# Kernel tuning notes

Hardware: AMD Instinct MI355X
Metric: run time of the kernel (lower is better)

The kernel has to match this reference:

```python
import jax, jax.numpy as jnp
import numpy as np

EMBED_DIM = 1024
NUM_HEADS = 16
HEAD_DIM = EMBED_DIM // NUM_HEADS


def setup_inputs() -> dict:
    key = jax.random.key(0)
    k1, k2, k3, k4 = jax.random.split(key, 4)
    B, N, C = 4, 4096, EMBED_DIM
    x = jax.random.normal(k1, (B, N, C), dtype=jnp.float32)
    scale = 1.0 / np.sqrt(C)
    W_qkv = jax.random.normal(k2, (C, 3 * C), dtype=jnp.float32) * scale
    W_out = jax.random.normal(k3, (C, C), dtype=jnp.float32) * scale
    b_out = jax.random.normal(k4, (C,), dtype=jnp.float32) * 0.01
    return {"x": x, "W_qkv": W_qkv, "W_out": W_out, "b_out": b_out}


def reference(x, W_qkv, W_out, b_out):
    B, N, C = x.shape
    H, D = NUM_HEADS, HEAD_DIM
    qkv = (x @ W_qkv).reshape(B, N, 3, H, D)
    qkv = jnp.transpose(qkv, (2, 0, 3, 1, 4))  # (3, B, H, N, D)
    q, k, v = qkv[0], qkv[1], qkv[2]
    q = jax.nn.elu(q) + 1.0
    k = jax.nn.elu(k) + 1.0
    kv = jnp.einsum('bhnd,bhne->bhde', k, v)          # (B,H,D,D)
    num = jnp.einsum('bhnd,bhde->bhne', q, kv)        # (B,H,N,D)
    normalizer = jnp.einsum('bhnd,bhd->bhn', q, k.sum(axis=2))
    out = num / (normalizer[..., None] + 1e-6)
    out = jnp.transpose(out, (0, 2, 1, 3)).reshape(B, N, C)
    return out @ W_out + b_out
```

## Files before the change

### kernel.cpp

```cpp
#include <hip/hip_runtime.h>
#include <hip/hip_bf16.h>

using bf16x8 = __bf16 __attribute__((ext_vector_type(8)));
using f32x4  = float  __attribute__((ext_vector_type(4)));
using u16x8  = unsigned short __attribute__((ext_vector_type(8)));
using u16x4  = unsigned short __attribute__((ext_vector_type(4)));

__device__ __forceinline__ unsigned short f2bf(float f) {
  unsigned u = __builtin_bit_cast(unsigned, f);
  u += 0x7fffu + ((u >> 16) & 1u);
  return (unsigned short)(u >> 16);
}
__device__ __forceinline__ float bf2f(unsigned short h) {
  return __builtin_bit_cast(float, (unsigned)h << 16);
}

__device__ __forceinline__ void gload16(const void* g, void* l) {
  __builtin_amdgcn_global_load_lds(
      (const __attribute__((address_space(1))) void*)g,
      (__attribute__((address_space(3))) void*)l, 16, 0, 0);
}

__device__ __forceinline__ void barrier_raw() {
  asm volatile("" ::: "memory");
  __builtin_amdgcn_s_barrier();
  asm volatile("" ::: "memory");
}
#define LGKM0() asm volatile("s_waitcnt lgkmcnt(0)" ::: "memory")
#define VMC6()  asm volatile("s_waitcnt vmcnt(6)" ::: "memory")
#define VMC0()  asm volatile("s_waitcnt vmcnt(0)" ::: "memory")

__global__ __launch_bounds__(256) void conv_f32_bf16(const float* __restrict__ in,
                                                     unsigned short* __restrict__ out, int n) {
  int stride = gridDim.x * 256 * 4;
  for (int i = (blockIdx.x * 256 + threadIdx.x) * 4; i < n; i += stride) {
    float4 v = *reinterpret_cast<const float4*>(in + i);
    u16x4 o = { f2bf(v.x), f2bf(v.y), f2bf(v.z), f2bf(v.w) };
    *reinterpret_cast<u16x4*>(out + i) = o;
  }
}

__global__ __launch_bounds__(256) void transpose_f32_bf16(const float* __restrict__ in,
                                                          unsigned short* __restrict__ out,
                                                          int R, int C) {
  __shared__ float t[64][65];
  int c0 = blockIdx.x * 64, r0 = blockIdx.y * 64;
  int lx = threadIdx.x & 63, ly = threadIdx.x >> 6;
#pragma unroll
  for (int i = 0; i < 16; ++i) {
    int r = ly * 16 + i;
    t[r][lx] = in[(size_t)(r0 + r) * C + c0 + lx];
  }
  __syncthreads();
#pragma unroll
  for (int i = 0; i < 16; ++i) {
    int c = ly * 16 + i;
    out[(size_t)(c0 + c) * R + r0 + lx] = f2bf(t[lx][c]);
  }
}

__device__ __forceinline__ void gemm256_mainloop(
    const unsigned short* __restrict__ A, const unsigned short* __restrict__ Bt,
    int brow, int bcol, char* lds, f32x4 (&acc)[8][4]) {
  constexpr int NT = 16;
  const int tid  = threadIdx.x;
  const int lane = tid & 63;
  const int w    = tid >> 6;
  const int wr   = w >> 2, wc = w & 3;
  const int lr   = lane & 15, kg = lane >> 4;

  const int o0 = tid * 16;
  const int o1 = 8192 + tid * 16;
  const int p0 = o0 ^ (((o0 >> 7) & 7) << 4);
  const int p1 = o1 ^ (((o1 >> 7) & 7) << 4);
  const int off0 = (p0 >> 7) * 2048 + (p0 & 127);
  const int off1 = (p1 >> 7) * 2048 + (p1 & 127);
  const int wq = w << 10;

  const int xr  = (lr & 7) << 4;
  const int ck0 = (kg * 16) ^ xr;
  const int ck1 = (64 + kg * 16) ^ xr;
  const int aoff = wr * 16384 + lr * 128;
  const int boff = 32768 + (wc >> 1) * 16384 + (wc & 1) * 8192 + lr * 128;

  auto STAGE = [&](const unsigned short* G, int rowbase, int t, int region) {
    const char* gb = (const char*)(G + (size_t)rowbase * 1024 + t * 64);
    char* lb = lds + region + wq;
    gload16(gb + off0, lb);
    gload16(gb + off1, lb + 8192);
  };

  STAGE(Bt, bcol,       0, 32768);
  STAGE(Bt, bcol + 128, 0, 32768 + 16384);
  STAGE(A,  brow,       0, 0);
  STAGE(A,  brow + 128, 0, 16384);
  STAGE(Bt, bcol,       1, 65536 + 32768);
  STAGE(Bt, bcol + 128, 1, 65536 + 32768 + 16384);
  STAGE(A,  brow,       1, 65536);
  VMC6();
  barrier_raw();

  bf16x8 aF[4][2], bF[4][2];
  for (int t = 0; t < NT; ++t) {
    const int bufo  = (t & 1) << 16;
    const int nbufo = bufo ^ 65536;
    const char* LA = lds + bufo + aoff;
    const char* LB = lds + bufo + boff;

#pragma unroll
    for (int n = 0; n < 2; ++n) {
      bF[n][0] = __builtin_bit_cast(bf16x8, *(const u16x8*)(LB + n * 2048 + ck0));
      bF[n][1] = __builtin_bit_cast(bf16x8, *(const u16x8*)(LB + n * 2048 + ck1));
    }
#pragma unroll
    for (int m = 0; m < 4; ++m) {
      aF[m][0] = __builtin_bit_cast(bf16x8, *(const u16x8*)(LA + m * 2048 + ck0));
      aF[m][1] = __builtin_bit_cast(bf16x8, *(const u16x8*)(LA + m * 2048 + ck1));
    }
    if (t + 1 < NT) STAGE(A, brow + 128, t + 1, nbufo + 16384);
    barrier_raw();
    LGKM0();
    __builtin_amdgcn_s_setprio(1);
#pragma unroll
    for (int kk = 0; kk < 2; ++kk)
#pragma unroll
      for (int m = 0; m < 4; ++m)
#pragma unroll
        for (int n = 0; n < 2; ++n)
          acc[m][n] = __builtin_amdgcn_mfma_f32_16x16x32_bf16(aF[m][kk], bF[n][kk], acc[m][n], 0, 0, 0);
    __builtin_amdgcn_s_setprio(0);
    barrier_raw();

#pragma unroll
    for (int n = 2; n < 4; ++n) {
      bF[n][0] = __builtin_bit_cast(bf16x8, *(const u16x8*)(LB + n * 2048 + ck0));
      bF[n][1] = __builtin_bit_cast(bf16x8, *(const u16x8*)(LB + n * 2048 + ck1));
    }
    barrier_raw();
    LGKM0();
    __builtin_amdgcn_s_setprio(1);
#pragma unroll
    for (int kk = 0; kk < 2; ++kk)
#pragma unroll
      for (int m = 0; m < 4; ++m)
#pragma unroll
        for (int n = 2; n < 4; ++n)
          acc[m][n] = __builtin_amdgcn_mfma_f32_16x16x32_bf16(aF[m][kk], bF[n][kk], acc[m][n], 0, 0, 0);
    __builtin_amdgcn_s_setprio(0);
    barrier_raw();

#pragma unroll
    for (int m = 0; m < 4; ++m) {
      aF[m][0] = __builtin_bit_cast(bf16x8, *(const u16x8*)(LA + (m + 4) * 2048 + ck0));
      aF[m][1] = __builtin_bit_cast(bf16x8, *(const u16x8*)(LA + (m + 4) * 2048 + ck1));
    }
    if (t + 2 < NT) STAGE(Bt, bcol, t + 2, bufo + 32768);
    barrier_raw();
    LGKM0();
    __builtin_amdgcn_s_setprio(1);
#pragma unroll
    for (int kk = 0; kk < 2; ++kk)
#pragma unroll
      for (int m = 0; m < 4; ++m)
#pragma unroll
        for (int n = 2; n < 4; ++n)
          acc[m + 4][n] = __builtin_amdgcn_mfma_f32_16x16x32_bf16(aF[m][kk], bF[n][kk], acc[m + 4][n], 0, 0, 0);
    __builtin_amdgcn_s_setprio(0);
    barrier_raw();

    if (t + 2 < NT) {
      STAGE(Bt, bcol + 128, t + 2, bufo + 32768 + 16384);
      STAGE(A,  brow,       t + 2, bufo);
    }
    barrier_raw();
    __builtin_amdgcn_s_setprio(1);
#pragma unroll
    for (int kk = 0; kk < 2; ++kk)
#pragma unroll
      for (int m = 0; m < 4; ++m)
#pragma unroll
        for (int n = 0; n < 2; ++n)
          acc[m + 4][n] = __builtin_amdgcn_mfma_f32_16x16x32_bf16(aF[m][kk], bF[n][kk], acc[m + 4][n], 0, 0, 0);
    __builtin_amdgcn_s_setprio(0);
    if (t + 2 < NT) { VMC6(); } else { VMC0(); }
    barrier_raw();
  }
}

__global__ __launch_bounds__(512, 2) void gemm_qkv(
    const unsigned short* __restrict__ xbf, const unsigned short* __restrict__ wt,
    unsigned short* __restrict__ q, unsigned short* __restrict__ k, unsigned short* __restrict__ v) {
  __shared__ __align__(16) char lds[131072];
  f32x4 acc[8][4] = {};
  const int bid = blockIdx.x;
  const int r = bid & 7, i = bid >> 3;
  const int tm = r * 8 + (i & 7);
  const int tn = i >> 3;
  const int brow = tm * 256, bcol = tn * 256;
  gemm256_mainloop(xbf, wt, brow, bcol, lds, acc);

  const int lane = threadIdx.x & 63, w = threadIdx.x >> 6;
  const int wr = w >> 2, wc = w & 3;
  const int lr = lane & 15, kg = lane >> 4;
#pragma unroll
  for (int m = 0; m < 8; ++m)
#pragma unroll
    for (int n = 0; n < 4; ++n)
#pragma unroll
      for (int rr = 0; rr < 4; ++rr) {
        int grow = brow + wr * 128 + m * 16 + kg * 4 + rr;
        int gcol = bcol + wc * 64 + n * 16 + lr;
        float val = acc[m][n][rr];
        int tt = gcol >> 10;
        int h = (gcol >> 6) & 15;
        int d = gcol & 63;
        int b = grow >> 12, s = grow & 4095;
        size_t idx = ((size_t)(b * 16 + h) * 4096 + s) * 64 + d;
        if (tt < 2) {
          val = val > 0.f ? val + 1.f : __expf(val);
          (tt == 0 ? q : k)[idx] = f2bf(val);
        } else {
          v[idx] = f2bf(val);
        }
      }
}

__global__ __launch_bounds__(512, 2) void gemm_out(
    const unsigned short* __restrict__ attn, const unsigned short* __restrict__ wt,
    const float* __restrict__ bias, float* __restrict__ out) {
  __shared__ __align__(16) char lds[131072];
  f32x4 acc[8][4] = {};
  const int bid = blockIdx.x;
  const int r = bid & 7, i = bid >> 3;
  const int tm = r * 8 + (i & 7);
  const int tn = i >> 3;
  const int brow = tm * 256, bcol = tn * 256;
  gemm256_mainloop(attn, wt, brow, bcol, lds, acc);

  const int lane = threadIdx.x & 63, w = threadIdx.x >> 6;
  const int wr = w >> 2, wc = w & 3;
  const int lr = lane & 15, kg = lane >> 4;
#pragma unroll
  for (int m = 0; m < 8; ++m)
#pragma unroll
    for (int n = 0; n < 4; ++n)
#pragma unroll
      for (int rr = 0; rr < 4; ++rr) {
        int grow = brow + wr * 128 + m * 16 + kg * 4 + rr;
        int gcol = bcol + wc * 64 + n * 16 + lr;
        out[(size_t)grow * 1024 + gcol] = acc[m][n][rr] + bias[gcol];
      }
}

__global__ __launch_bounds__(256) void kv_kernel(
    const unsigned short* __restrict__ k, const unsigned short* __restrict__ v,
    float* __restrict__ kv, float* __restrict__ ksum) {
  const int bid = blockIdx.x;
  const int bh = bid >> 3, chunk = bid & 7;
  const unsigned short* kb = k + (size_t)bh * 4096 * 64 + chunk * 512 * 64;
  const unsigned short* vb = v + (size_t)bh * 4096 * 64 + chunk * 512 * 64;
  __shared__ unsigned short ks[64 * 64];
  __shared__ unsigned short vs[64 * 64];
  const int tid = threadIdx.x;
  const int ty = tid >> 4, tx = tid & 15;
  float acc[4][4] = {};
  float ksacc[4] = {};
  for (int t = 0; t < 8; ++t) {
    const unsigned short* ksrc = kb + t * 4096;
    const unsigned short* vsrc = vb + t * 4096;
    *reinterpret_cast<u16x8*>(&ks[tid * 8])        = *reinterpret_cast<const u16x8*>(ksrc + tid * 8);
    *reinterpret_cast<u16x8*>(&ks[2048 + tid * 8]) = *reinterpret_cast<const u16x8*>(ksrc + 2048 + tid * 8);
    *reinterpret_cast<u16x8*>(&vs[tid * 8])        = *reinterpret_cast<const u16x8*>(vsrc + tid * 8);
    *reinterpret_cast<u16x8*>(&vs[2048 + tid * 8]) = *reinterpret_cast<const u16x8*>(vsrc + 2048 + tid * 8);
    __syncthreads();
#pragma unroll 4
    for (int nn = 0; nn < 64; ++nn) {
      u16x4 ku = *reinterpret_cast<const u16x4*>(&ks[nn * 64 + ty * 4]);
      u16x4 vu = *reinterpret_cast<const u16x4*>(&vs[nn * 64 + tx * 4]);
      float kd[4], ve[4];
#pragma unroll
      for (int i = 0; i < 4; ++i) { kd[i] = bf2f(ku[i]); ve[i] = bf2f(vu[i]); }
#pragma unroll
      for (int i = 0; i < 4; ++i) ksacc[i] += kd[i];
#pragma unroll
      for (int i = 0; i < 4; ++i)
#pragma unroll
        for (int j = 0; j < 4; ++j) acc[i][j] += kd[i] * ve[j];
    }
    __syncthreads();
  }
  float* kvb = kv + (size_t)bh * 4096;
#pragma unroll
  for (int i = 0; i < 4; ++i)
#pragma unroll
    for (int j = 0; j < 4; ++j)
      atomicAdd(&kvb[(tx * 4 + j) * 64 + ty * 4 + i], acc[i][j]);
  if (tx == 0) {
#pragma unroll
    for (int i = 0; i < 4; ++i) atomicAdd(&ksum[bh * 64 + ty * 4 + i], ksacc[i]);
  }
}

__global__ __launch_bounds__(256) void num_kernel(
    const unsigned short* __restrict__ q, const float* __restrict__ kv,
    const float* __restrict__ ksum, unsigned short* __restrict__ attn) {
  const int bid = blockIdx.x;
  const int bh = bid >> 6, sblk = bid & 63;
  const int b = bh >> 4, h = bh & 15;
  __shared__ unsigned short kvs[64 * 72];
  __shared__ float ksum_s[64];
  __shared__ float norm_s[64];
  const int tid = threadIdx.x;
  const float* kvb = kv + (size_t)bh * 4096;
#pragma unroll
  for (int r = 0; r < 4; ++r) {
    int e = r * 1024 + tid * 4;
    float4 f = *reinterpret_cast<const float4*>(&kvb[e]);
    int row = e >> 6, col = e & 63;
    u16x4 o = { f2bf(f.x), f2bf(f.y), f2bf(f.z), f2bf(f.w) };
    *reinterpret_cast<u16x4*>(&kvs[row * 72 + col]) = o;
  }
  if (tid < 16) {
    float4 f = *reinterpret_cast<const float4*>(&ksum[bh * 64 + tid * 4]);
    ksum_s[tid * 4 + 0] = f.x; ksum_s[tid * 4 + 1] = f.y;
    ksum_s[tid * 4 + 2] = f.z; ksum_s[tid * 4 + 3] = f.w;
  }
  __syncthreads();

  const int lane = tid & 63, w = tid >> 6;
  const int lr = lane & 15, kg = lane >> 4;
  const int s0 = sblk * 64 + w * 16;
  const unsigned short* qrow = q + ((size_t)bh * 4096 + s0 + lr) * 64 + kg * 8;
  u16x8 a0u = *reinterpret_cast<const u16x8*>(qrow);
  u16x8 a1u = *reinterpret_cast<const u16x8*>(qrow + 32);
  bf16x8 a0 = __builtin_bit_cast(bf16x8, a0u);
  bf16x8 a1 = __builtin_bit_cast(bf16x8, a1u);

  float p = 0.f;
#pragma unroll
  for (int j = 0; j < 8; ++j) {
    p += bf2f(a0u[j]) * ksum_s[kg * 8 + j];
    p += bf2f(a1u[j]) * ksum_s[32 + kg * 8 + j];
  }
  p += __shfl_xor(p, 16);
  p += __shfl_xor(p, 32);
  if (kg == 0) norm_s[w * 16 + lr] = p;

  f32x4 accs[4];
#pragma unroll
  for (int jf = 0; jf < 4; ++jf) {
    u16x8 b0u = *reinterpret_cast<const u16x8*>(&kvs[(jf * 16 + lr) * 72 + kg * 8]);
    u16x8 b1u = *reinterpret_cast<const u16x8*>(&kvs[(jf * 16 + lr) * 72 + 32 + kg * 8]);
    f32x4 c = {0.f, 0.f, 0.f, 0.f};
    c = __builtin_amdgcn_mfma_f32_16x16x32_bf16(a0, __builtin_bit_cast(bf16x8, b0u), c, 0, 0, 0);
    c = __builtin_amdgcn_mfma_f32_16x16x32_bf16(a1, __builtin_bit_cast(bf16x8, b1u), c, 0, 0, 0);
    accs[jf] = c;
  }
  float dn[4];
#pragma unroll
  for (int r = 0; r < 4; ++r) dn[r] = norm_s[w * 16 + kg * 4 + r] + 1e-6f;

  unsigned short* ab = attn + (size_t)b * 4096 * 1024 + h * 64;
#pragma unroll
  for (int jf = 0; jf < 4; ++jf)
#pragma unroll
    for (int r = 0; r < 4; ++r) {
      int s = s0 + kg * 4 + r;
      int e2 = jf * 16 + lr;
      ab[(size_t)s * 1024 + e2] = f2bf(accs[jf][r] / dn[r]);
    }
}

extern "C" void kernel_launch(void* const* d_in, const int* in_sizes, int n_in,
                              void* d_out, int out_size, void* d_ws, size_t ws_size,
                              hipStream_t stream) {
  const float* x     = (const float*)d_in[0];
  const float* W_qkv = (const float*)d_in[1];
  const float* W_out = (const float*)d_in[2];
  const float* b_out = (const float*)d_in[3];
  float* out = (float*)d_out;

  unsigned short* xbf   = (unsigned short*)d_ws;
  unsigned short* attnb = xbf;
  unsigned short* wqkvT = xbf + 16777216;
  unsigned short* woutT = wqkvT + 3145728;
  unsigned short* qb    = woutT + 1048576;
  unsigned short* kb    = qb + 16777216;
  unsigned short* vb    = kb + 16777216;
  float* kvw            = (float*)(vb + 16777216);
  float* ksumw          = kvw + 262144;

  conv_f32_bf16<<<2048, 256, 0, stream>>>(x, xbf, 16777216);
  transpose_f32_bf16<<<dim3(48, 16), 256, 0, stream>>>(W_qkv, wqkvT, 1024, 3072);
  transpose_f32_bf16<<<dim3(16, 16), 256, 0, stream>>>(W_out, woutT, 1024, 1024);
  hipMemsetAsync(kvw, 0, (262144 + 4096) * sizeof(float), stream);
  gemm_qkv<<<768, 512, 0, stream>>>(xbf, wqkvT, qb, kb, vb);
  kv_kernel<<<512, 256, 0, stream>>>(kb, vb, kvw, ksumw);
  num_kernel<<<4096, 256, 0, stream>>>(qb, kvw, ksumw, attnb);
  gemm_out<<<256, 512, 0, stream>>>(attnb, woutT, b_out, out);
}
```

Measured before the change: 261.2 us.

## Restructure GEMM mainloop into two-barrier ping-pong schedule with register double-buffering

```diff
diff --git a/kernel.cpp b/kernel.cpp
--- a/kernel.cpp
+++ b/kernel.cpp
@@ -26,9 +26,8 @@
   __builtin_amdgcn_s_barrier();
   asm volatile("" ::: "memory");
 }
-#define LGKM0() asm volatile("s_waitcnt lgkmcnt(0)" ::: "memory")
-#define VMC6()  asm volatile("s_waitcnt vmcnt(6)" ::: "memory")
-#define VMC0()  asm volatile("s_waitcnt vmcnt(0)" ::: "memory")
+#define VMC4() asm volatile("s_waitcnt vmcnt(4)" ::: "memory")
+#define VMC0() asm volatile("s_waitcnt vmcnt(0)" ::: "memory")
 
 __global__ __launch_bounds__(256) void conv_f32_bf16(const float* __restrict__ in,
                                                      unsigned short* __restrict__ out, int n) {
@@ -90,100 +89,84 @@
     gload16(gb + off1, lb + 8192);
   };
 
+  bf16x8 aQ[4][2], aR[4][2], bL0[2][2], bL1[2][2], bH[2][2];
+
+  auto READ_A = [&](bf16x8 (&dst)[4][2], int bufo, int mb) {
+#pragma unroll
+    for (int m = 0; m < 4; ++m) {
+      const char* p = lds + bufo + aoff + (mb + m) * 2048;
+      dst[m][0] = __builtin_bit_cast(bf16x8, *(const u16x8*)(p + ck0));
+      dst[m][1] = __builtin_bit_cast(bf16x8, *(const u16x8*)(p + ck1));
+    }
+  };
+  auto READ_B = [&](bf16x8 (&dst)[2][2], int bufo, int nb) {
+#pragma unroll
+    for (int n = 0; n < 2; ++n) {
+      const char* p = lds + bufo + boff + (nb + n) * 2048;
+      dst[n][0] = __builtin_bit_cast(bf16x8, *(const u16x8*)(p + ck0));
+      dst[n][1] = __builtin_bit_cast(bf16x8, *(const u16x8*)(p + ck1));
+    }
+  };
+  auto MFMA_Q = [&](int mb, int nb, bf16x8 (&Af)[4][2], bf16x8 (&Bf)[2][2]) {
+    __builtin_amdgcn_s_setprio(1);
+#pragma unroll
+    for (int kk = 0; kk < 2; ++kk)
+#pragma unroll
+      for (int m = 0; m < 4; ++m)
+#pragma unroll
+        for (int n = 0; n < 2; ++n)
+          acc[mb + m][nb + n] =
+              __builtin_amdgcn_mfma_f32_16x16x32_bf16(Af[m][kk], Bf[n][kk], acc[mb + m][nb + n], 0, 0, 0);
+    __builtin_amdgcn_s_setprio(0);
+  };
+
   STAGE(Bt, bcol,       0, 32768);
-  STAGE(Bt, bcol + 128, 0, 32768 + 16384);
+  STAGE(Bt, bcol + 128, 0, 49152);
   STAGE(A,  brow,       0, 0);
   STAGE(A,  brow + 128, 0, 16384);
   STAGE(Bt, bcol,       1, 65536 + 32768);
-  STAGE(Bt, bcol + 128, 1, 65536 + 32768 + 16384);
-  STAGE(A,  brow,       1, 65536);
-  VMC6();
+  STAGE(Bt, bcol + 128, 1, 65536 + 49152);
+  VMC4();
   barrier_raw();
-
-  bf16x8 aF[4][2], bF[4][2];
-  for (int t = 0; t < NT; ++t) {
-    const int bufo  = (t & 1) << 16;
-    const int nbufo = bufo ^ 65536;
-    const char* LA = lds + bufo + aoff;
-    const char* LB = lds + bufo + boff;
-
-#pragma unroll
-    for (int n = 0; n < 2; ++n) {
-      bF[n][0] = __builtin_bit_cast(bf16x8, *(const u16x8*)(LB + n * 2048 + ck0));
-      bF[n][1] = __builtin_bit_cast(bf16x8, *(const u16x8*)(LB + n * 2048 + ck1));
-    }
-#pragma unroll
-    for (int m = 0; m < 4; ++m) {
-      aF[m][0] = __builtin_bit_cast(bf16x8, *(const u16x8*)(LA + m * 2048 + ck0));
-      aF[m][1] = __builtin_bit_cast(bf16x8, *(const u16x8*)(LA + m * 2048 + ck1));
-    }
-    if (t + 1 < NT) STAGE(A, brow + 128, t + 1, nbufo + 16384);
+  READ_A(aQ, 0, 0);
+  READ_B(bL0, 0, 0);
+
+  for (int t = 0; t < NT; t += 2) {
+    if (t + 1 < NT) { STAGE(A, brow, t + 1, 65536); STAGE(A, brow + 128, t + 1, 65536 + 16384); }
+    READ_B(bH, 0, 2);
+    MFMA_Q(0, 0, aQ, bL0);
+    READ_A(aR, 0, 4);
+    MFMA_Q(0, 2, aQ, bH);
+    MFMA_Q(4, 2, aR, bH);
     barrier_raw();
-    LGKM0();
-    __builtin_amdgcn_s_setprio(1);
-#pragma unroll
-    for (int kk = 0; kk < 2; ++kk)
-#pragma unroll
-      for (int m = 0; m < 4; ++m)
-#pragma unroll
-        for (int n = 0; n < 2; ++n)
-          acc[m][n] = __builtin_amdgcn_mfma_f32_16x16x32_bf16(aF[m][kk], bF[n][kk], acc[m][n], 0, 0, 0);
-    __builtin_amdgcn_s_setprio(0);
+    if (t + 2 < NT) {
+      STAGE(Bt, bcol, t + 2, 32768); STAGE(Bt, bcol + 128, t + 2, 49152);
+      VMC4();
+    } else if (t + 1 < NT) {
+      VMC0();
+    }
     barrier_raw();
-
-#pragma unroll
-    for (int n = 2; n < 4; ++n) {
-      bF[n][0] = __builtin_bit_cast(bf16x8, *(const u16x8*)(LB + n * 2048 + ck0));
-      bF[n][1] = __builtin_bit_cast(bf16x8, *(const u16x8*)(LB + n * 2048 + ck1));
-    }
-    barrier_raw();
-    LGKM0();
-    __builtin_amdgcn_s_setprio(1);
-#pragma unroll
-    for (int kk = 0; kk < 2; ++kk)
-#pragma unroll
-      for (int m = 0; m < 4; ++m)
-#pragma unroll
-        for (int n = 2; n < 4; ++n)
-          acc[m][n] = __builtin_amdgcn_mfma_f32_16x16x32_bf16(aF[m][kk], bF[n][kk], acc[m][n], 0, 0, 0);
-    __builtin_amdgcn_s_setprio(0);
-    barrier_raw();
-
-#pragma unroll
-    for (int m = 0; m < 4; ++m) {
-      aF[m][0] = __builtin_bit_cast(bf16x8, *(const u16x8*)(LA + (m + 4) * 2048 + ck0));
-      aF[m][1] = __builtin_bit_cast(bf16x8, *(const u16x8*)(LA + (m + 4) * 2048 + ck1));
-    }
-    if (t + 2 < NT) STAGE(Bt, bcol, t + 2, bufo + 32768);
-    barrier_raw();
-    LGKM0();
-    __builtin_amdgcn_s_setprio(1);
-#pragma unroll
-    for (int kk = 0; kk < 2; ++kk)
-#pragma unroll
-      for (int m = 0; m < 4; ++m)
-#pragma unroll
-        for (int n = 2; n < 4; ++n)
-          acc[m + 4][n] = __builtin_amdgcn_mfma_f32_16x16x32_bf16(aF[m][kk], bF[n][kk], acc[m + 4][n], 0, 0, 0);
-    __builtin_amdgcn_s_setprio(0);
-    barrier_raw();
-
-    if (t + 2 < NT) {
-      STAGE(Bt, bcol + 128, t + 2, bufo + 32768 + 16384);
-      STAGE(A,  brow,       t + 2, bufo);
-    }
-    barrier_raw();
-    __builtin_amdgcn_s_setprio(1);
-#pragma unroll
-    for (int kk = 0; kk < 2; ++kk)
-#pragma unroll
-      for (int m = 0; m < 4; ++m)
-#pragma unroll
-        for (int n = 0; n < 2; ++n)
-          acc[m + 4][n] = __builtin_amdgcn_mfma_f32_16x16x32_bf16(aF[m][kk], bF[n][kk], acc[m + 4][n], 0, 0, 0);
-    __builtin_amdgcn_s_setprio(0);
-    if (t + 2 < NT) { VMC6(); } else { VMC0(); }
-    barrier_raw();
+    if (t + 1 < NT) { READ_A(aQ, 65536, 0); READ_B(bL1, 65536, 0); }
+    MFMA_Q(4, 0, aR, bL0);
+
+    if (t + 1 < NT) {
+      if (t + 2 < NT) { STAGE(A, brow, t + 2, 0); STAGE(A, brow + 128, t + 2, 16384); }
+      READ_B(bH, 65536, 2);
+      MFMA_Q(0, 0, aQ, bL1);
+      READ_A(aR, 65536, 4);
+      MFMA_Q(0, 2, aQ, bH);
+      MFMA_Q(4, 2, aR, bH);
+      barrier_raw();
+      if (t + 3 < NT) {
+        STAGE(Bt, bcol, t + 3, 65536 + 32768); STAGE(Bt, bcol + 128, t + 3, 65536 + 49152);
+        VMC4();
+      } else if (t + 2 < NT) {
+        VMC0();
+      }
+      barrier_raw();
+      if (t + 2 < NT) { READ_A(aQ, 0, 0); READ_B(bL0, 0, 0); }
+      MFMA_Q(4, 0, aR, bL1);
+    }
   }
 }
 
```

Result: slower. 320.0 us (+22.5%).

## Compute K^T V with MFMA and write partial sums instead of atomics

Applied to the files above, without the earlier changes.

```diff
diff --git a/kernel.cpp b/kernel.cpp
--- a/kernel.cpp
+++ b/kernel.cpp
@@ -91,11 +91,11 @@
   };
 
   STAGE(Bt, bcol,       0, 32768);
-  STAGE(Bt, bcol + 128, 0, 32768 + 16384);
+  STAGE(Bt, bcol + 128, 0, 49152);
   STAGE(A,  brow,       0, 0);
   STAGE(A,  brow + 128, 0, 16384);
   STAGE(Bt, bcol,       1, 65536 + 32768);
-  STAGE(Bt, bcol + 128, 1, 65536 + 32768 + 16384);
+  STAGE(Bt, bcol + 128, 1, 65536 + 49152);
   STAGE(A,  brow,       1, 65536);
   VMC6();
   barrier_raw();
@@ -169,7 +169,7 @@
     barrier_raw();
 
     if (t + 2 < NT) {
-      STAGE(Bt, bcol + 128, t + 2, bufo + 32768 + 16384);
+      STAGE(Bt, bcol + 128, t + 2, bufo + 49152);
       STAGE(A,  brow,       t + 2, bufo);
     }
     barrier_raw();
@@ -252,58 +252,93 @@
       }
 }
 
-__global__ __launch_bounds__(256) void kv_kernel(
+__global__ __launch_bounds__(256) void kv_mfma(
     const unsigned short* __restrict__ k, const unsigned short* __restrict__ v,
-    float* __restrict__ kv, float* __restrict__ ksum) {
+    float* __restrict__ kv_part, float* __restrict__ ksum_part) {
   const int bid = blockIdx.x;
-  const int bh = bid >> 3, chunk = bid & 7;
-  const unsigned short* kb = k + (size_t)bh * 4096 * 64 + chunk * 512 * 64;
-  const unsigned short* vb = v + (size_t)bh * 4096 * 64 + chunk * 512 * 64;
-  __shared__ unsigned short ks[64 * 64];
-  __shared__ unsigned short vs[64 * 64];
-  const int tid = threadIdx.x;
-  const int ty = tid >> 4, tx = tid & 15;
-  float acc[4][4] = {};
-  float ksacc[4] = {};
-  for (int t = 0; t < 8; ++t) {
-    const unsigned short* ksrc = kb + t * 4096;
-    const unsigned short* vsrc = vb + t * 4096;
-    *reinterpret_cast<u16x8*>(&ks[tid * 8])        = *reinterpret_cast<const u16x8*>(ksrc + tid * 8);
-    *reinterpret_cast<u16x8*>(&ks[2048 + tid * 8]) = *reinterpret_cast<const u16x8*>(ksrc + 2048 + tid * 8);
-    *reinterpret_cast<u16x8*>(&vs[tid * 8])        = *reinterpret_cast<const u16x8*>(vsrc + tid * 8);
-    *reinterpret_cast<u16x8*>(&vs[2048 + tid * 8]) = *reinterpret_cast<const u16x8*>(vsrc + 2048 + tid * 8);
+  const int bh = bid >> 1, half = bid & 1;
+  const size_t nbase = (size_t)bh * 4096 + half * 2048;
+  __shared__ unsigned short kt[64 * 72];
+  __shared__ unsigned short vt[64 * 72];
+  const int tid  = threadIdx.x;
+  const int lane = tid & 63, w = tid >> 6;
+  const int lr = lane & 15, kg = lane >> 4;
+  const int srow = w * 16 + (lane >> 2);
+  const int sd   = (lane & 3) * 16;
+
+  f32x4 acc[4] = {{0.f,0.f,0.f,0.f},{0.f,0.f,0.f,0.f},{0.f,0.f,0.f,0.f},{0.f,0.f,0.f,0.f}};
+  f32x4 ks[4]  = {{0.f,0.f,0.f,0.f},{0.f,0.f,0.f,0.f},{0.f,0.f,0.f,0.f},{0.f,0.f,0.f,0.f}};
+  const u16x8 onesu = { 0x3F80,0x3F80,0x3F80,0x3F80,0x3F80,0x3F80,0x3F80,0x3F80 };
+  const bf16x8 aone = __builtin_bit_cast(bf16x8, onesu);
+
+  const int arow = w * 16 + lr;
+  const int axor = ((arow >> 3) & 7) << 3;
+  const unsigned short* aB[2];
+  aB[0] = vt + arow * 72 + ((kg * 8) ^ axor);
+  aB[1] = vt + arow * 72 + ((32 + kg * 8) ^ axor);
+  const unsigned short* bB[4][2];
+#pragma unroll
+  for (int dt = 0; dt < 4; ++dt) {
+    int drow = dt * 16 + lr;
+    int dxor = ((drow >> 3) & 7) << 3;
+    bB[dt][0] = kt + drow * 72 + ((kg * 8) ^ dxor);
+    bB[dt][1] = kt + drow * 72 + ((32 + kg * 8) ^ dxor);
+  }
+
+  u16x8 pk0, pk1, pv0, pv1;
+  auto LOADR = [&](int sub) {
+    const unsigned short* kr = k + (nbase + (size_t)sub * 64 + srow) * 64 + sd;
+    const unsigned short* vr = v + (nbase + (size_t)sub * 64 + srow) * 64 + sd;
+    pk0 = *(const u16x8*)kr;  pk1 = *(const u16x8*)(kr + 8);
+    pv0 = *(const u16x8*)vr;  pv1 = *(const u16x8*)(vr + 8);
+  };
+  LOADR(0);
+
+  for (int sub = 0; sub < 32; ++sub) {
     __syncthreads();
-#pragma unroll 4
-    for (int nn = 0; nn < 64; ++nn) {
-      u16x4 ku = *reinterpret_cast<const u16x4*>(&ks[nn * 64 + ty * 4]);
-      u16x4 vu = *reinterpret_cast<const u16x4*>(&vs[nn * 64 + tx * 4]);
-      float kd[4], ve[4];
-#pragma unroll
-      for (int i = 0; i < 4; ++i) { kd[i] = bf2f(ku[i]); ve[i] = bf2f(vu[i]); }
-#pragma unroll
-      for (int i = 0; i < 4; ++i) ksacc[i] += kd[i];
-#pragma unroll
-      for (int i = 0; i < 4; ++i)
-#pragma unroll
-        for (int j = 0; j < 4; ++j) acc[i][j] += kd[i] * ve[j];
-    }
+    u16x8 k0 = pk0, k1 = pk1, v0 = pv0, v1 = pv1;
+#pragma unroll
+    for (int j = 0; j < 8; ++j) {
+      int d0 = sd + j, d1 = sd + 8 + j;
+      int x0 = ((d0 >> 3) & 7) << 3, x1 = ((d1 >> 3) & 7) << 3;
+      kt[d0 * 72 + (srow ^ x0)] = k0[j];
+      kt[d1 * 72 + (srow ^ x1)] = k1[j];
+      vt[d0 * 72 + (srow ^ x0)] = v0[j];
+      vt[d1 * 72 + (srow ^ x1)] = v1[j];
+    }
+    if (sub + 1 < 32) LOADR(sub + 1);
     __syncthreads();
-  }
-  float* kvb = kv + (size_t)bh * 4096;
-#pragma unroll
-  for (int i = 0; i < 4; ++i)
-#pragma unroll
-    for (int j = 0; j < 4; ++j)
-      atomicAdd(&kvb[(tx * 4 + j) * 64 + ty * 4 + i], acc[i][j]);
-  if (tx == 0) {
-#pragma unroll
-    for (int i = 0; i < 4; ++i) atomicAdd(&ksum[bh * 64 + ty * 4 + i], ksacc[i]);
+#pragma unroll
+    for (int kk = 0; kk < 2; ++kk) {
+      bf16x8 af = __builtin_bit_cast(bf16x8, *(const u16x8*)aB[kk]);
+#pragma unroll
+      for (int dt = 0; dt < 4; ++dt) {
+        bf16x8 bf = __builtin_bit_cast(bf16x8, *(const u16x8*)bB[dt][kk]);
+        acc[dt] = __builtin_amdgcn_mfma_f32_16x16x32_bf16(af, bf, acc[dt], 0, 0, 0);
+        if (w == 0)
+          ks[dt] = __builtin_amdgcn_mfma_f32_16x16x32_bf16(aone, bf, ks[dt], 0, 0, 0);
+      }
+    }
+  }
+
+  float* kvp = kv_part + ((size_t)half * 128 + bh) * 4096;
+#pragma unroll
+  for (int dt = 0; dt < 4; ++dt)
+#pragma unroll
+    for (int r = 0; r < 4; ++r) {
+      int e = w * 16 + kg * 4 + r;
+      kvp[e * 64 + dt * 16 + lr] = acc[dt][r];
+    }
+  if (w == 0 && kg == 0) {
+    float* ksp = ksum_part + (size_t)half * 8192 + bh * 64;
+#pragma unroll
+    for (int dt = 0; dt < 4; ++dt) ksp[dt * 16 + lr] = ks[dt][0];
   }
 }
 
 __global__ __launch_bounds__(256) void num_kernel(
-    const unsigned short* __restrict__ q, const float* __restrict__ kv,
-    const float* __restrict__ ksum, unsigned short* __restrict__ attn) {
+    const unsigned short* __restrict__ q, const float* __restrict__ kv_part,
+    const float* __restrict__ ksum_part, unsigned short* __restrict__ attn) {
   const int bid = blockIdx.x;
   const int bh = bid >> 6, sblk = bid & 63;
   const int b = bh >> 4, h = bh & 15;
@@ -311,19 +346,23 @@
   __shared__ float ksum_s[64];
   __shared__ float norm_s[64];
   const int tid = threadIdx.x;
-  const float* kvb = kv + (size_t)bh * 4096;
+  const float* kv0 = kv_part + (size_t)bh * 4096;
+  const float* kv1 = kv_part + (size_t)(128 + bh) * 4096;
 #pragma unroll
   for (int r = 0; r < 4; ++r) {
     int e = r * 1024 + tid * 4;
-    float4 f = *reinterpret_cast<const float4*>(&kvb[e]);
+    float4 f0 = *reinterpret_cast<const float4*>(&kv0[e]);
+    float4 f1 = *reinterpret_cast<const float4*>(&kv1[e]);
+    float4 f = { f0.x + f1.x, f0.y + f1.y, f0.z + f1.z, f0.w + f1.w };
     int row = e >> 6, col = e & 63;
     u16x4 o = { f2bf(f.x), f2bf(f.y), f2bf(f.z), f2bf(f.w) };
     *reinterpret_cast<u16x4*>(&kvs[row * 72 + col]) = o;
   }
   if (tid < 16) {
-    float4 f = *reinterpret_cast<const float4*>(&ksum[bh * 64 + tid * 4]);
-    ksum_s[tid * 4 + 0] = f.x; ksum_s[tid * 4 + 1] = f.y;
-    ksum_s[tid * 4 + 2] = f.z; ksum_s[tid * 4 + 3] = f.w;
+    float4 f0 = *reinterpret_cast<const float4*>(&ksum_part[bh * 64 + tid * 4]);
+    float4 f1 = *reinterpret_cast<const float4*>(&ksum_part[8192 + bh * 64 + tid * 4]);
+    ksum_s[tid * 4 + 0] = f0.x + f1.x; ksum_s[tid * 4 + 1] = f0.y + f1.y;
+    ksum_s[tid * 4 + 2] = f0.z + f1.z; ksum_s[tid * 4 + 3] = f0.w + f1.w;
   }
   __syncthreads();
 
@@ -387,15 +426,14 @@
   unsigned short* qb    = woutT + 1048576;
   unsigned short* kb    = qb + 16777216;
   unsigned short* vb    = kb + 16777216;
-  float* kvw            = (float*)(vb + 16777216);
-  float* ksumw          = kvw + 262144;
+  float* kvp            = (float*)(vb + 16777216);
+  float* ksp            = kvp + 1048576;
 
   conv_f32_bf16<<<2048, 256, 0, stream>>>(x, xbf, 16777216);
   transpose_f32_bf16<<<dim3(48, 16), 256, 0, stream>>>(W_qkv, wqkvT, 1024, 3072);
   transpose_f32_bf16<<<dim3(16, 16), 256, 0, stream>>>(W_out, woutT, 1024, 1024);
-  hipMemsetAsync(kvw, 0, (262144 + 4096) * sizeof(float), stream);
   gemm_qkv<<<768, 512, 0, stream>>>(xbf, wqkvT, qb, kb, vb);
-  kv_kernel<<<512, 256, 0, stream>>>(kb, vb, kvw, ksumw);
-  num_kernel<<<4096, 256, 0, stream>>>(qb, kvw, ksumw, attnb);
+  kv_mfma<<<256, 256, 0, stream>>>(kb, vb, kvp, ksp);
+  num_kernel<<<4096, 256, 0, stream>>>(qb, kvp, ksp, attnb);
   gemm_out<<<256, 512, 0, stream>>>(attnb, woutT, b_out, out);
 }
```

Result: faster. 237.6 us (-9.0%).
